# Kernel tuning notes

Measured on AMD Instinct MI355X. Metric: run time of the kernel, lower is better.

Reference implementation:

```python
import jax, jax.numpy as jnp
import numpy as np

E = 1024      # embed_dim
H = 16        # num_heads
D = E // H    # head_dim
SCALING = float(D * 1.0) ** (-0.5)


def setup_inputs() -> dict:
    key = jax.random.key(0)
    ks = jax.random.split(key, 10)
    B, L, S = 4, 2048, 2048
    query = jax.random.normal(ks[0], (B, L, E), dtype=jnp.float32)
    k_in = jax.random.normal(ks[1], (B, S, E), dtype=jnp.float32)
    v_in = jax.random.normal(ks[2], (B, S, E), dtype=jnp.float32)
    attn_bias = jax.random.normal(ks[3], (L, S), dtype=jnp.float32)
    attn_mask = jax.random.normal(ks[4], (L, S), dtype=jnp.float32)
    # in_proj: Linear(E, 3E)  (xavier-uniform-ish scale), out_proj: Linear(E, E)
    lim_in = np.sqrt(6.0 / (E + 3 * E))
    Wqkv = jax.random.uniform(ks[5], (3 * E, E), minval=-lim_in, maxval=lim_in, dtype=jnp.float32)
    bqkv = jnp.zeros((3 * E,), dtype=jnp.float32)
    lim_out = np.sqrt(1.0 / E)
    Wo = jax.random.uniform(ks[6], (E, E), minval=-lim_out, maxval=lim_out, dtype=jnp.float32)
    bo = jnp.zeros((E,), dtype=jnp.float32)
    return {"query": query, "key": k_in, "value": v_in,
            "attn_bias": attn_bias, "attn_mask": attn_mask,
            "Wqkv": Wqkv, "bqkv": bqkv, "Wo": Wo, "bo": bo}


def reference(query, key, value, attn_bias, attn_mask, Wqkv, bqkv, Wo, bo):
    B, L, _ = query.shape
    S = key.shape[1]
    # fused in_proj split into q/k/v slices (q from query, k from key, v from value)
    q = query @ Wqkv[:E].T + bqkv[:E]
    k = key @ Wqkv[E:2 * E].T + bqkv[E:2 * E]
    v = value @ Wqkv[2 * E:].T + bqkv[2 * E:]
    q = q * SCALING
    # [B, L, H, D]
    q = q.reshape(B, L, H, D)
    k = k.reshape(B, S, H, D)
    v = v.reshape(B, S, H, D)
    # scores: [B, H, L, S] with additive float mask and bias (broadcast over B, H)
    scores = jnp.einsum("blhd,bshd->bhls", q, k)
    scores = scores + attn_mask[None, None] + attn_bias[None, None]
    weights = jax.nn.softmax(scores, axis=-1)  # dropout p=0.0 -> identity
    out = jnp.einsum("bhls,bshd->blhd", weights, v).reshape(B, L, E)
    return out @ Wo.T + bo
```

## Files before the change

### kernel.cpp

```cpp
#include <hip/hip_runtime.h>
#include <hip/hip_bf16.h>

#define BB 4
#define LL 2048
#define SS 2048
#define EE 1024
#define HH 16
#define DD 64
#define MM (BB * LL)
#define LOG2E 1.44269504088896340736f

typedef unsigned short u16;
typedef u16   u16x4  __attribute__((ext_vector_type(4)));
typedef u16   u16x8  __attribute__((ext_vector_type(8)));
typedef float f32x4  __attribute__((ext_vector_type(4)));
typedef __bf16 bf16x4 __attribute__((ext_vector_type(4)));
typedef __bf16 bf16x8 __attribute__((ext_vector_type(8)));

__device__ __forceinline__ u16 f2bf(float x) {
    unsigned u = __float_as_uint(x);
    u += 0x7fffu + ((u >> 16) & 1u);
    return (u16)(u >> 16);
}
__device__ __forceinline__ float bf2f(u16 b) {
    return __uint_as_float(((unsigned)b) << 16);
}

__device__ __forceinline__ void gload16(const u16* g, u16* l) {
    __builtin_amdgcn_global_load_lds(
        (const __attribute__((address_space(1))) void*)g,
        (__attribute__((address_space(3))) void*)l, 16, 0, 0);
}

__global__ __launch_bounds__(256) void f32_to_bf16_kernel(
    const float* __restrict__ in, u16* __restrict__ out)
{
    size_t idx = ((size_t)blockIdx.x * 256 + threadIdx.x) * 8;
    f32x4 a = *(const f32x4*)(in + idx);
    f32x4 b = *(const f32x4*)(in + idx + 4);
    u16x8 o;
#pragma unroll
    for (int j = 0; j < 4; j++) { o[j] = f2bf(a[j]); o[4 + j] = f2bf(b[j]); }
    *(u16x8*)(out + idx) = o;
}

__global__ __launch_bounds__(256) void combine_bias_kernel(
    const float* __restrict__ bias, const float* __restrict__ mask,
    u16* __restrict__ comb)
{
    int idx = (blockIdx.x * 256 + threadIdx.x) * 8;
    f32x4 a0 = *(const f32x4*)(bias + idx);
    f32x4 a1 = *(const f32x4*)(bias + idx + 4);
    f32x4 m0 = *(const f32x4*)(mask + idx);
    f32x4 m1 = *(const f32x4*)(mask + idx + 4);
    u16x8 o;
#pragma unroll
    for (int j = 0; j < 4; j++) {
        o[j]     = f2bf((a0[j] + m0[j]) * LOG2E);
        o[4 + j] = f2bf((a1[j] + m1[j]) * LOG2E);
    }
    *(u16x8*)(comb + idx) = o;
}

template <int OUTBF16>
__global__ __launch_bounds__(256, 2) void gemm_bt_bf16(
    const u16* __restrict__ A, const u16* __restrict__ Bw,
    const float* __restrict__ bias, void* __restrict__ Cp,
    int M, int N, int K, float scale)
{
    __shared__ __align__(16) u16 As[128 * 64];
    __shared__ __align__(16) u16 Bs[128 * 64];
    const int tid = threadIdx.x;
    const int lane = tid & 63, wave = tid >> 6;
    const int quad = lane >> 4, ln = lane & 15;
    const int wm = (wave & 1) * 64, wn = (wave >> 1) * 64;
    const int m0 = blockIdx.x * 128, n0 = blockIdx.y * 128;

    const int r8 = lane >> 3, c8 = lane & 7;
    const u16* Ag = A  + (size_t)m0 * K + c8 * 8;
    const u16* Bg = Bw + (size_t)n0 * K + c8 * 8;

    f32x4 acc[4][4];
#pragma unroll
    for (int mt = 0; mt < 4; mt++)
#pragma unroll
        for (int nt = 0; nt < 4; nt++) acc[mt][nt] = (f32x4){0.f, 0.f, 0.f, 0.f};

    for (int k0 = 0; k0 < K; k0 += 64) {
        __syncthreads();
#pragma unroll
        for (int i = 0; i < 4; i++) {
            int ch = i * 4 + wave;
            int row = ch * 8 + r8;
            gload16(Ag + (size_t)row * K + k0, &As[ch * 512]);
            gload16(Bg + (size_t)row * K + k0, &Bs[ch * 512]);
        }
        __syncthreads();

#pragma unroll
        for (int ks = 0; ks < 2; ks++) {
            bf16x8 af[4], bfg[4];
#pragma unroll
            for (int mt = 0; mt < 4; mt++)
                af[mt] = *(const bf16x8*)(&As[(wm + mt * 16 + ln) * 64 + ks * 32 + quad * 8]);
#pragma unroll
            for (int nt = 0; nt < 4; nt++)
                bfg[nt] = *(const bf16x8*)(&Bs[(wn + nt * 16 + ln) * 64 + ks * 32 + quad * 8]);
#pragma unroll
            for (int mt = 0; mt < 4; mt++)
#pragma unroll
                for (int nt = 0; nt < 4; nt++)
                    acc[mt][nt] = __builtin_amdgcn_mfma_f32_16x16x32_bf16(
                        af[mt], bfg[nt], acc[mt][nt], 0, 0, 0);
        }
    }

#pragma unroll
    for (int nt = 0; nt < 4; nt++) {
        int n = n0 + wn + nt * 16 + ln;
        float bn = bias[n];
#pragma unroll
        for (int mt = 0; mt < 4; mt++) {
#pragma unroll
            for (int r = 0; r < 4; r++) {
                int m = m0 + wm + mt * 16 + quad * 4 + r;
                float val = (acc[mt][nt][r] + bn) * scale;
                if (OUTBF16) ((u16*)Cp)[(size_t)m * N + n] = f2bf(val);
                else         ((float*)Cp)[(size_t)m * N + n] = val;
            }
        }
    }
}

__global__ __launch_bounds__(256) void transpose_v_kernel(
    const u16* __restrict__ vb, u16* __restrict__ vt)
{
    __shared__ __align__(16) u16 t[64 * 72];
    const int bh = blockIdx.y, b = bh >> 4, h = bh & 15;
    const int s0 = blockIdx.x * 64;
    const int tid = threadIdx.x;
#pragma unroll
    for (int i = 0; i < 2; i++) {
        int chunk = tid + 256 * i;
        int row = chunk >> 3, c = chunk & 7;
        u16x8 v = *(const u16x8*)(vb + (size_t)(b * SS + s0 + row) * EE + h * 64 + c * 8);
        *(u16x8*)(t + row * 72 + c * 8) = v;
    }
    __syncthreads();
#pragma unroll
    for (int i = 0; i < 2; i++) {
        int chunk = tid + 256 * i;
        int d = chunk >> 3, c = chunk & 7;
        u16x8 o;
#pragma unroll
        for (int j = 0; j < 8; j++) o[j] = t[(c * 8 + j) * 72 + d];
        *(u16x8*)(vt + (size_t)(bh * 64 + d) * SS + s0 + c * 8) = o;
    }
}

__global__ __launch_bounds__(256, 2) void attn_kernel(
    const u16* __restrict__ qb,
    const u16* __restrict__ kb,
    const u16* __restrict__ vt,
    const u16* __restrict__ comb,
    u16* __restrict__ attn)
{
    __shared__ __align__(16) u16 KPs[128 * 136];
    __shared__ __align__(16) u16 Vs[64 * 136];
    const int tid = threadIdx.x, lane = tid & 63, wave = tid >> 6;
    const int quad = lane >> 4, ln = lane & 15;
    const int bh = blockIdx.y, b = bh >> 4, h = bh & 15;
    const int q0 = blockIdx.x * 128;
    const int qloc0 = wave * 32;

    bf16x8 qf[2][2];
#pragma unroll
    for (int qg = 0; qg < 2; qg++)
#pragma unroll
        for (int ks = 0; ks < 2; ks++)
            qf[qg][ks] = *(const bf16x8*)(qb + (size_t)(b * LL + q0 + qloc0 + 16 * qg + ln) * EE
                                          + h * 64 + ks * 32 + quad * 8);

    const u16* cb0 = comb + (size_t)(q0 + qloc0 + ln) * SS + quad * 4;
    const u16* cb1 = cb0 + (size_t)16 * SS;

    f32x4 o[4][2];
#pragma unroll
    for (int mt = 0; mt < 4; mt++) { o[mt][0] = (f32x4){0,0,0,0}; o[mt][1] = (f32x4){0,0,0,0}; }
    f32x4 ls0 = (f32x4){0,0,0,0}, ls1 = (f32x4){0,0,0,0};

    u16x8 kreg[4], vreg[4];
    auto load_kv = [&](int s0) {
#pragma unroll
        for (int i = 0; i < 4; i++) {
            int chunk = tid + 256 * i, row = chunk >> 3, c = chunk & 7;
            kreg[i] = *(const u16x8*)(kb + (size_t)(b * SS + s0 + row) * EE + h * 64 + c * 8);
        }
#pragma unroll
        for (int i = 0; i < 4; i++) {
            int chunk = tid + 256 * i, row = chunk >> 4, c = chunk & 15;
            vreg[i] = *(const u16x8*)(vt + (size_t)(bh * 64 + row) * SS + s0 + c * 8);
        }
    };
    load_kv(0);

    for (int s0 = 0; s0 < SS; s0 += 128) {
        __syncthreads();
#pragma unroll
        for (int i = 0; i < 4; i++) {
            int chunk = tid + 256 * i, row = chunk >> 3, c = chunk & 7;
            *(u16x8*)(KPs + row * 72 + c * 8) = kreg[i];
        }
#pragma unroll
        for (int i = 0; i < 4; i++) {
            int chunk = tid + 256 * i, row = chunk >> 4, c = chunk & 15;
            *(u16x8*)(Vs + row * 136 + c * 8) = vreg[i];
        }
        u16x4 bfr[8][2];
#pragma unroll
        for (int mt = 0; mt < 8; mt++) {
            bfr[mt][0] = *(const u16x4*)(cb0 + s0 + mt * 16);
            bfr[mt][1] = *(const u16x4*)(cb1 + s0 + mt * 16);
        }
        __syncthreads();

        if (s0 + 128 < SS) load_kv(s0 + 128);

        f32x4 st[8][2];
#pragma unroll
        for (int mt = 0; mt < 8; mt++)
#pragma unroll
            for (int r = 0; r < 4; r++) {
                st[mt][0][r] = bf2f(bfr[mt][0][r]);
                st[mt][1][r] = bf2f(bfr[mt][1][r]);
            }

        __builtin_amdgcn_s_setprio(1);
#pragma unroll
        for (int mt = 0; mt < 8; mt++) {
            bf16x8 a0 = *(const bf16x8*)(KPs + (mt * 16 + ln) * 72 + quad * 8);
            bf16x8 a1 = *(const bf16x8*)(KPs + (mt * 16 + ln) * 72 + 32 + quad * 8);
            st[mt][0] = __builtin_amdgcn_mfma_f32_16x16x32_bf16(a0, qf[0][0], st[mt][0], 0, 0, 0);
            st[mt][0] = __builtin_amdgcn_mfma_f32_16x16x32_bf16(a1, qf[0][1], st[mt][0], 0, 0, 0);
            st[mt][1] = __builtin_amdgcn_mfma_f32_16x16x32_bf16(a0, qf[1][0], st[mt][1], 0, 0, 0);
            st[mt][1] = __builtin_amdgcn_mfma_f32_16x16x32_bf16(a1, qf[1][1], st[mt][1], 0, 0, 0);
        }
        __builtin_amdgcn_s_setprio(0);

        bf16x4 p[8][2];
#pragma unroll
        for (int mt = 0; mt < 8; mt++)
#pragma unroll
            for (int r = 0; r < 4; r++) {
                float e0 = __builtin_amdgcn_exp2f(st[mt][0][r]);
                float e1 = __builtin_amdgcn_exp2f(st[mt][1][r]);
                ls0[r] += e0; ls1[r] += e1;
                p[mt][0][r] = (__bf16)e0;
                p[mt][1][r] = (__bf16)e1;
            }

        __syncthreads();

#pragma unroll
        for (int mt = 0; mt < 8; mt++) {
            *(bf16x4*)(KPs + (qloc0 + ln) * 136 + mt * 16 + quad * 4)      = p[mt][0];
            *(bf16x4*)(KPs + (qloc0 + 16 + ln) * 136 + mt * 16 + quad * 4) = p[mt][1];
        }

#pragma unroll
        for (int ks = 0; ks < 4; ks++) {
            bf16x8 pf0 = *(const bf16x8*)(KPs + (qloc0 + ln) * 136 + ks * 32 + quad * 8);
            bf16x8 pf1 = *(const bf16x8*)(KPs + (qloc0 + 16 + ln) * 136 + ks * 32 + quad * 8);
            __builtin_amdgcn_s_setprio(1);
#pragma unroll
            for (int mt = 0; mt < 4; mt++) {
                bf16x8 a = *(const bf16x8*)(Vs + (mt * 16 + ln) * 136 + ks * 32 + quad * 8);
                o[mt][0] = __builtin_amdgcn_mfma_f32_16x16x32_bf16(a, pf0, o[mt][0], 0, 0, 0);
                o[mt][1] = __builtin_amdgcn_mfma_f32_16x16x32_bf16(a, pf1, o[mt][1], 0, 0, 0);
            }
            __builtin_amdgcn_s_setprio(0);
        }
    }

    float lsum0 = (ls0[0] + ls0[1]) + (ls0[2] + ls0[3]);
    float lsum1 = (ls1[0] + ls1[1]) + (ls1[2] + ls1[3]);
    lsum0 += __shfl_xor(lsum0, 16); lsum0 += __shfl_xor(lsum0, 32);
    lsum1 += __shfl_xor(lsum1, 16); lsum1 += __shfl_xor(lsum1, 32);
    float inv0 = 1.f / lsum0, inv1 = 1.f / lsum1;

#pragma unroll
    for (int mt = 0; mt < 4; mt++) {
        bf16x4 p0, p1;
#pragma unroll
        for (int r = 0; r < 4; r++) {
            p0[r] = (__bf16)(o[mt][0][r] * inv0);
            p1[r] = (__bf16)(o[mt][1][r] * inv1);
        }
        *(bf16x4*)(KPs + (qloc0 + ln) * 136 + mt * 16 + quad * 4)      = p0;
        *(bf16x4*)(KPs + (qloc0 + 16 + ln) * 136 + mt * 16 + quad * 4) = p1;
    }
#pragma unroll
    for (int i = 0; i < 4; i++) {
        int j = lane + 64 * i;
        int r = j >> 3, c = j & 7;
        u16x8 v = *(const u16x8*)(KPs + (qloc0 + r) * 136 + c * 8);
        *(u16x8*)(attn + (size_t)(b * LL + q0 + qloc0 + r) * EE + h * 64 + c * 8) = v;
    }
}

extern "C" void kernel_launch(void* const* d_in, const int* in_sizes, int n_in,
                              void* d_out, int out_size, void* d_ws, size_t ws_size,
                              hipStream_t stream)
{
    (void)in_sizes; (void)n_in; (void)out_size; (void)ws_size;
    const float* query     = (const float*)d_in[0];
    const float* key       = (const float*)d_in[1];
    const float* value     = (const float*)d_in[2];
    const float* attn_bias = (const float*)d_in[3];
    const float* attn_mask = (const float*)d_in[4];
    const float* Wqkv      = (const float*)d_in[5];
    const float* bqkv      = (const float*)d_in[6];
    const float* Wo        = (const float*)d_in[7];
    const float* bo        = (const float*)d_in[8];
    float* out = (float*)d_out;

    u16* wq_bf = (u16*)d_ws;
    u16* wo_bf = wq_bf + 3 * EE * EE;
    u16* comb  = wo_bf + EE * EE;
    u16* q_bf  = comb + (size_t)LL * SS;
    u16* k_bf  = q_bf + (size_t)MM * EE;
    u16* v_bf  = k_bf + (size_t)MM * EE;
    u16* vtr   = v_bf + (size_t)MM * EE;
    u16* attnb = vtr  + (size_t)MM * EE;
    u16* tmp   = attnb;

    f32_to_bf16_kernel<<<3 * EE * EE / 2048, 256, 0, stream>>>(Wqkv, wq_bf);
    f32_to_bf16_kernel<<<EE * EE / 2048, 256, 0, stream>>>(Wo, wo_bf);
    combine_bias_kernel<<<(LL * SS) / 2048, 256, 0, stream>>>(attn_bias, attn_mask, comb);

    dim3 gg(MM / 128, EE / 128);
    f32_to_bf16_kernel<<<(int)((size_t)MM * EE / 2048), 256, 0, stream>>>(query, tmp);
    gemm_bt_bf16<1><<<gg, 256, 0, stream>>>(tmp, wq_bf,              bqkv,          q_bf, MM, EE, EE, 0.125f * LOG2E);
    f32_to_bf16_kernel<<<(int)((size_t)MM * EE / 2048), 256, 0, stream>>>(key, tmp);
    gemm_bt_bf16<1><<<gg, 256, 0, stream>>>(tmp, wq_bf + EE * EE,     bqkv + EE,     k_bf, MM, EE, EE, 1.f);
    f32_to_bf16_kernel<<<(int)((size_t)MM * EE / 2048), 256, 0, stream>>>(value, tmp);
    gemm_bt_bf16<1><<<gg, 256, 0, stream>>>(tmp, wq_bf + 2 * EE * EE, bqkv + 2 * EE, v_bf, MM, EE, EE, 1.f);

    transpose_v_kernel<<<dim3(SS / 64, BB * HH), 256, 0, stream>>>(v_bf, vtr);

    attn_kernel<<<dim3(LL / 128, BB * HH), 256, 0, stream>>>(q_bf, k_bf, vtr, comb, attnb);

    gemm_bt_bf16<0><<<gg, 256, 0, stream>>>(attnb, wo_bf, bo, out, MM, EE, EE, 1.f);
}
```

Before: 454.9 us.

## Fuse fp32-to-bf16 conversion and V transpose into projection GEMMs, remap block order

The Q/K/V projection GEMMs now read fp32 activations directly, convert them to bf16 in registers, and prefetch the next K-tile while computing. This removes three separate conversion kernels and their round trips through memory. The V projection writes its output already transposed through an LDS staging tile, so the standalone transpose kernel is gone. Both the GEMM and attention grids use a 1D block-index swizzle to improve L2 locality, at the cost of more register pressure and a padded LDS A-tile in the fused GEMM.

```diff
diff --git a/kernel.cpp b/kernel.cpp
--- a/kernel.cpp
+++ b/kernel.cpp
@@ -62,23 +62,31 @@
     *(u16x8*)(comb + idx) = o;
 }
 
-template <int OUTBF16>
-__global__ __launch_bounds__(256, 2) void gemm_bt_bf16(
-    const u16* __restrict__ A, const u16* __restrict__ Bw,
+template <int ABF16, int OUTBF16, int VOUT>
+__global__ __launch_bounds__(256, 2) void gemm_bt(
+    const void* __restrict__ Ap, const u16* __restrict__ Bw,
     const float* __restrict__ bias, void* __restrict__ Cp,
     int M, int N, int K, float scale)
 {
-    __shared__ __align__(16) u16 As[128 * 64];
-    __shared__ __align__(16) u16 Bs[128 * 64];
+    __shared__ __align__(16) u16 SH[128 * 72 + 128 * 64];
+    constexpr int ASTR = ABF16 ? 64 : 72;
+    u16* As = SH;
+    u16* Bs = SH + 128 * ASTR;
+    u16* Tr = SH;
+
     const int tid = threadIdx.x;
     const int lane = tid & 63, wave = tid >> 6;
     const int quad = lane >> 4, ln = lane & 15;
     const int wm = (wave & 1) * 64, wn = (wave >> 1) * 64;
-    const int m0 = blockIdx.x * 128, n0 = blockIdx.y * 128;
+
+    const int bid = blockIdx.x;
+    const int vid = (bid & 7) * 8 + ((bid >> 3) & 7) + (bid >> 6) * 64;
+    const int m0 = (vid >> 3) * 128, n0 = (vid & 7) * 128;
 
     const int r8 = lane >> 3, c8 = lane & 7;
-    const u16* Ag = A  + (size_t)m0 * K + c8 * 8;
-    const u16* Bg = Bw + (size_t)n0 * K + c8 * 8;
+    const float* Af = (const float*)Ap;
+    const u16*   Ab = (const u16*)Ap + (size_t)m0 * K + c8 * 8;
+    const u16*   Bg = Bw + (size_t)n0 * K + c8 * 8;
 
     f32x4 acc[4][4];
 #pragma unroll
@@ -86,23 +94,51 @@
 #pragma unroll
         for (int nt = 0; nt < 4; nt++) acc[mt][nt] = (f32x4){0.f, 0.f, 0.f, 0.f};
 
-    for (int k0 = 0; k0 < K; k0 += 64) {
+    f32x4 apf[8];
+
+    auto load_a = [&](int k0) {
+        if (!ABF16) {
+#pragma unroll
+            for (int i = 0; i < 8; i++) {
+                int chunk = tid + 256 * i, row = chunk >> 4, c = chunk & 15;
+                apf[i] = *(const f32x4*)(Af + (size_t)(m0 + row) * K + k0 + c * 4);
+            }
+        }
+    };
+
+    load_a(0);
+
+    const int KT = K >> 6;
+    for (int kt = 0; kt < KT; kt++) {
+        const int k0 = kt << 6;
         __syncthreads();
 #pragma unroll
         for (int i = 0; i < 4; i++) {
             int ch = i * 4 + wave;
             int row = ch * 8 + r8;
-            gload16(Ag + (size_t)row * K + k0, &As[ch * 512]);
             gload16(Bg + (size_t)row * K + k0, &Bs[ch * 512]);
-        }
-        __syncthreads();
+            if (ABF16) gload16(Ab + (size_t)row * K + k0, &As[ch * 512]);
+        }
+        if (!ABF16) {
+#pragma unroll
+            for (int i = 0; i < 8; i++) {
+                int chunk = tid + 256 * i, row = chunk >> 4, c = chunk & 15;
+                u16x4 o;
+#pragma unroll
+                for (int j = 0; j < 4; j++) o[j] = f2bf(apf[i][j]);
+                *(u16x4*)(As + row * ASTR + c * 4) = o;
+            }
+        }
+        __syncthreads();
+
+        if (kt + 1 < KT) load_a(k0 + 64);
 
 #pragma unroll
         for (int ks = 0; ks < 2; ks++) {
             bf16x8 af[4], bfg[4];
 #pragma unroll
             for (int mt = 0; mt < 4; mt++)
-                af[mt] = *(const bf16x8*)(&As[(wm + mt * 16 + ln) * 64 + ks * 32 + quad * 8]);
+                af[mt] = *(const bf16x8*)(&As[(wm + mt * 16 + ln) * ASTR + ks * 32 + quad * 8]);
 #pragma unroll
             for (int nt = 0; nt < 4; nt++)
                 bfg[nt] = *(const bf16x8*)(&Bs[(wn + nt * 16 + ln) * 64 + ks * 32 + quad * 8]);
@@ -115,46 +151,48 @@
         }
     }
 
-#pragma unroll
-    for (int nt = 0; nt < 4; nt++) {
-        int n = n0 + wn + nt * 16 + ln;
-        float bn = bias[n];
-#pragma unroll
-        for (int mt = 0; mt < 4; mt++) {
-#pragma unroll
-            for (int r = 0; r < 4; r++) {
-                int m = m0 + wm + mt * 16 + quad * 4 + r;
-                float val = (acc[mt][nt][r] + bn) * scale;
-                if (OUTBF16) ((u16*)Cp)[(size_t)m * N + n] = f2bf(val);
-                else         ((float*)Cp)[(size_t)m * N + n] = val;
-            }
-        }
-    }
-}
-
-__global__ __launch_bounds__(256) void transpose_v_kernel(
-    const u16* __restrict__ vb, u16* __restrict__ vt)
-{
-    __shared__ __align__(16) u16 t[64 * 72];
-    const int bh = blockIdx.y, b = bh >> 4, h = bh & 15;
-    const int s0 = blockIdx.x * 64;
-    const int tid = threadIdx.x;
-#pragma unroll
-    for (int i = 0; i < 2; i++) {
-        int chunk = tid + 256 * i;
-        int row = chunk >> 3, c = chunk & 7;
-        u16x8 v = *(const u16x8*)(vb + (size_t)(b * SS + s0 + row) * EE + h * 64 + c * 8);
-        *(u16x8*)(t + row * 72 + c * 8) = v;
-    }
-    __syncthreads();
-#pragma unroll
-    for (int i = 0; i < 2; i++) {
-        int chunk = tid + 256 * i;
-        int d = chunk >> 3, c = chunk & 7;
-        u16x8 o;
-#pragma unroll
-        for (int j = 0; j < 8; j++) o[j] = t[(c * 8 + j) * 72 + d];
-        *(u16x8*)(vt + (size_t)(bh * 64 + d) * SS + s0 + c * 8) = o;
+    if (VOUT) {
+        __syncthreads();
+#pragma unroll
+        for (int nt = 0; nt < 4; nt++) {
+            int nl = wn + nt * 16 + ln;
+            float bn = bias[n0 + nl];
+#pragma unroll
+            for (int mt = 0; mt < 4; mt++)
+#pragma unroll
+                for (int r = 0; r < 4; r++) {
+                    int ml = wm + mt * 16 + quad * 4 + r;
+                    Tr[nl * 136 + ml] = f2bf(acc[mt][nt][r] + bn);
+                }
+        }
+        __syncthreads();
+        const int bq = m0 >> 11;
+        const int s0 = m0 & 2047;
+#pragma unroll
+        for (int i = 0; i < 8; i++) {
+            int chunk = tid + 256 * i;
+            int row = chunk >> 4, c = chunk & 15;
+            u16x8 v = *(const u16x8*)(Tr + row * 136 + c * 8);
+            int n = n0 + row;
+            int h = n >> 6, d = n & 63;
+            *(u16x8*)(((u16*)Cp) + ((size_t)((bq * 16 + h) * 64 + d)) * SS + s0 + c * 8) = v;
+        }
+    } else {
+#pragma unroll
+        for (int nt = 0; nt < 4; nt++) {
+            int n = n0 + wn + nt * 16 + ln;
+            float bn = bias[n];
+#pragma unroll
+            for (int mt = 0; mt < 4; mt++) {
+#pragma unroll
+                for (int r = 0; r < 4; r++) {
+                    int m = m0 + wm + mt * 16 + quad * 4 + r;
+                    float val = (acc[mt][nt][r] + bn) * scale;
+                    if (OUTBF16) ((u16*)Cp)[(size_t)m * N + n] = f2bf(val);
+                    else         ((float*)Cp)[(size_t)m * N + n] = val;
+                }
+            }
+        }
     }
 }
 
@@ -169,8 +207,11 @@
     __shared__ __align__(16) u16 Vs[64 * 136];
     const int tid = threadIdx.x, lane = tid & 63, wave = tid >> 6;
     const int quad = lane >> 4, ln = lane & 15;
-    const int bh = blockIdx.y, b = bh >> 4, h = bh & 15;
-    const int q0 = blockIdx.x * 128;
+
+    const int bid = blockIdx.x;
+    const int vid = (bid & 7) * 128 + (bid >> 3);
+    const int bh = vid >> 4, b = bh >> 4, h = bh & 15;
+    const int q0 = (vid & 15) * 128;
     const int qloc0 = wave * 32;
 
     bf16x8 qf[2][2];
@@ -332,23 +373,16 @@
     u16* v_bf  = k_bf + (size_t)MM * EE;
     u16* vtr   = v_bf + (size_t)MM * EE;
     u16* attnb = vtr  + (size_t)MM * EE;
-    u16* tmp   = attnb;
 
     f32_to_bf16_kernel<<<3 * EE * EE / 2048, 256, 0, stream>>>(Wqkv, wq_bf);
     f32_to_bf16_kernel<<<EE * EE / 2048, 256, 0, stream>>>(Wo, wo_bf);
     combine_bias_kernel<<<(LL * SS) / 2048, 256, 0, stream>>>(attn_bias, attn_mask, comb);
 
-    dim3 gg(MM / 128, EE / 128);
-    f32_to_bf16_kernel<<<(int)((size_t)MM * EE / 2048), 256, 0, stream>>>(query, tmp);
-    gemm_bt_bf16<1><<<gg, 256, 0, stream>>>(tmp, wq_bf,              bqkv,          q_bf, MM, EE, EE, 0.125f * LOG2E);
-    f32_to_bf16_kernel<<<(int)((size_t)MM * EE / 2048), 256, 0, stream>>>(key, tmp);
-    gemm_bt_bf16<1><<<gg, 256, 0, stream>>>(tmp, wq_bf + EE * EE,     bqkv + EE,     k_bf, MM, EE, EE, 1.f);
-    f32_to_bf16_kernel<<<(int)((size_t)MM * EE / 2048), 256, 0, stream>>>(value, tmp);
-    gemm_bt_bf16<1><<<gg, 256, 0, stream>>>(tmp, wq_bf + 2 * EE * EE, bqkv + 2 * EE, v_bf, MM, EE, EE, 1.f);
-
-    transpose_v_kernel<<<dim3(SS / 64, BB * HH), 256, 0, stream>>>(v_bf, vtr);
-
-    attn_kernel<<<dim3(LL / 128, BB * HH), 256, 0, stream>>>(q_bf, k_bf, vtr, comb, attnb);
-
-    gemm_bt_bf16<0><<<gg, 256, 0, stream>>>(attnb, wo_bf, bo, out, MM, EE, EE, 1.f);
-}
+    gemm_bt<0, 1, 0><<<512, 256, 0, stream>>>(query, wq_bf,               bqkv,          q_bf, MM, EE, EE, 0.125f * LOG2E);
+    gemm_bt<0, 1, 0><<<512, 256, 0, stream>>>(key,   wq_bf + EE * EE,     bqkv + EE,     k_bf, MM, EE, EE, 1.f);
+    gemm_bt<0, 1, 1><<<512, 256, 0, stream>>>(value, wq_bf + 2 * EE * EE, bqkv + 2 * EE, vtr,  MM, EE, EE, 1.f);
+
+    attn_kernel<<<1024, 256, 0, stream>>>(q_bf, k_bf, vtr, comb, attnb);
+
+    gemm_bt<1, 0, 0><<<512, 256, 0, stream>>>(attnb, wo_bf, bo, out, MM, EE, EE, 1.f);
+}
```

Measured after the change: 434.1 us. 4.6% less time.
